# Kernel tuning notes

Measured on AMD Instinct MI355X. Metric: run time of the kernel, lower is better.

Reference implementation:

```python
import jax, jax.numpy as jnp
import numpy as np

B, T, N = 32, 24, 512
DIM_IN, DIM_OUT, HID, EMB = 64, 2, 128, 16
NEG_SLOPE = 0.01  # nn.LeakyReLU default


def leaky_relu(x):
    return jnp.where(x >= 0, x, NEG_SLOPE * x)


def setup_inputs() -> dict:
    key = jax.random.key(0)
    ks = jax.random.split(key, 11)
    return {
        "eb": jax.random.normal(ks[0], (B, T, N, DIM_IN), jnp.float32),
        "time_eb": jax.random.normal(ks[1], (B, T, EMB), jnp.float32),
        "node_eb": jax.random.normal(ks[2], (N, EMB), jnp.float32),
        # ln1: Linear(dim_in, hidden) stored as [dim_in, hidden] (x @ W + b)
        "W1": jax.random.normal(ks[3], (DIM_IN, HID), jnp.float32) / np.sqrt(DIM_IN),
        "b1": jax.random.normal(ks[4], (HID,), jnp.float32) * 0.01,
        # ln3: Linear(hidden, dim_out)
        "W3": jax.random.normal(ks[5], (HID, DIM_OUT), jnp.float32) / np.sqrt(HID),
        "b3": jax.random.normal(ks[6], (DIM_OUT,), jnp.float32) * 0.01,
        "weights_pool_spa": jax.random.normal(ks[7], (EMB, HID, HID), jnp.float32),
        "bias_pool_spa": jax.random.normal(ks[8], (EMB, HID), jnp.float32),
        "weights_pool_tem": jax.random.normal(ks[9], (EMB, HID, HID), jnp.float32),
        "bias_pool_tem": jax.random.normal(ks[10], (EMB, HID), jnp.float32),
    }


def reference(eb, time_eb, node_eb, W1, b1, W3, b3,
              weights_pool_spa, bias_pool_spa,
              weights_pool_tem, bias_pool_tem):
    # eb: [b,t,n,dim_in] -> [b,t,n,hidden]
    eb_out = eb @ W1 + b1
    # spatial hypernetwork: per-node weight [n,hid,hid] and bias [n,hid]
    weights_spa = jnp.einsum('nd,dio->nio', node_eb, weights_pool_spa)
    bias_spa = node_eb @ bias_pool_spa  # [n,hid]
    out_spa = leaky_relu(jnp.einsum('btni,nio->btno', eb_out, weights_spa) + bias_spa)
    # temporal hypernetwork: per-(b,t) weight [b,t,hid,hid] and bias [b,t,1,hid]
    weights_tem = jnp.einsum('btd,dio->btio', time_eb, weights_pool_tem)
    bias_tem = (time_eb @ bias_pool_tem)[:, :, None, :]
    out_tem = leaky_relu(jnp.einsum('btni,btio->btno', out_spa, weights_tem) + bias_tem)
    logits = out_tem @ W3 + b3  # [b,t,n,dim_out]
    return logits
```

## Files before the change

### kernel.cpp

```cpp
#include <hip/hip_runtime.h>
#include <hip/hip_bf16.h>
#include <stdint.h>

#define BT   768
#define NN   512
#define DIN  64
#define HID  128
#define EMB  16
#define SLOPE 0.01f

typedef __attribute__((ext_vector_type(8))) short bf16x8;
typedef __attribute__((ext_vector_type(4))) float f32x4;
typedef __attribute__((ext_vector_type(4))) short short4v;

__device__ __forceinline__ short f2bf(float f) {
    uint32_t u = __float_as_uint(f);
    u += 0x7fff + ((u >> 16) & 1);
    return (short)(u >> 16);
}
__device__ __forceinline__ float bf2f(short s) {
    return __uint_as_float(((uint32_t)(unsigned short)s) << 16);
}

static const size_t OFF_WSPA = 0;
static const size_t OFF_WTEM = 16777216;
static const size_t OFF_BSPA = 41943040;
static const size_t OFF_BTEM = 42205184;
static const size_t OFF_PTS  = 42598400;
static const size_t OFF_PTT  = 43122688;
static const size_t OFF_W1T  = 43646976;
static const size_t OFF_H2   = 43663360;

__global__ __launch_bounds__(256)
void k_prep(const float* __restrict__ pool_spa, const float* __restrict__ pool_tem,
            const float* __restrict__ W1,
            const float* __restrict__ bp_spa, const float* __restrict__ bp_tem,
            const float* __restrict__ node_eb, const float* __restrict__ time_eb,
            short* __restrict__ pts, short* __restrict__ ptt,
            short* __restrict__ w1t, float* __restrict__ bspa,
            float* __restrict__ btem)
{
    const int b = blockIdx.x, t = threadIdx.x;
    if (b >= 129) {
        int q = (b - 129) * 256 + t;
        const float *bp, *emb; float* outp;
        if (q < NN * 32) { bp = bp_spa; emb = node_eb; outp = bspa; }
        else { q -= NN * 32; bp = bp_tem; emb = time_eb; outp = btem; }
        const int n = q >> 5, oq = q & 31;
        float4 a = make_float4(0.f, 0.f, 0.f, 0.f);
        #pragma unroll
        for (int d = 0; d < EMB; ++d) {
            float e = emb[n * EMB + d];
            float4 bv = ((const float4*)bp)[d * 32 + oq];
            a.x += e * bv.x; a.y += e * bv.y; a.z += e * bv.z; a.w += e * bv.w;
        }
        ((float4*)outp)[q] = a;
        return;
    }
    if (b == 128) {
        int o = t >> 1, kh = (t & 1) * 32;
        for (int k = 0; k < 32; ++k)
            w1t[o * 64 + kh + k] = f2bf(W1[(kh + k) * HID + o]);
        return;
    }
    const float* pool = (b < 64) ? pool_spa : pool_tem;
    short* outp = (b < 64) ? pts : ptt;
    const int bb = b & 63;
    const int d = bb >> 2, o0 = (bb & 3) * 32;
    __shared__ short s[32 * 136];
    #pragma unroll
    for (int c = 0; c < 16; ++c) {
        int e = c * 256 + t;
        int i = e >> 5, oo = e & 31;
        s[oo * 136 + i] = f2bf(pool[(d * HID + i) * HID + o0 + oo]);
    }
    __syncthreads();
    #pragma unroll
    for (int c = 0; c < 8; ++c) {
        int e = c * 256 + t;
        int oo = e >> 6, ii = (e & 63) * 2;
        uint32_t lo = (unsigned short)s[oo * 136 + ii];
        uint32_t hi = (unsigned short)s[oo * 136 + ii + 1];
        ((uint32_t*)outp)[((d * HID + o0 + oo) * HID + ii) >> 1] = lo | (hi << 16);
    }
}

__global__ __launch_bounds__(256)
void k_genw(const short* __restrict__ pts, const short* __restrict__ ptt,
            const float* __restrict__ node_eb, const float* __restrict__ time_eb,
            short* __restrict__ wspa, short* __restrict__ wtem)
{
    const int t = threadIdx.x;
    const bool spa = blockIdx.y < 8;
    const int nb = spa ? blockIdx.y : blockIdx.y - 8;
    const short* pool = spa ? pts : ptt;
    const float* emb = spa ? node_eb : time_eb;
    short* outp = spa ? wspa : wtem;
    __shared__ float sEmb[64 * EMB];
    #pragma unroll
    for (int c = 0; c < 4; ++c) {
        int idx = c * 256 + t;
        sEmb[idx] = emb[nb * 64 * EMB + idx];
    }
    __syncthreads();
    const int cq = blockIdx.x * 256 + t;
    float4 p[EMB];
    #pragma unroll
    for (int d = 0; d < EMB; ++d) {
        short4v v = ((const short4v*)pool)[d * 4096 + cq];
        p[d] = make_float4(bf2f(v.x), bf2f(v.y), bf2f(v.z), bf2f(v.w));
    }
    for (int nn = 0; nn < 64; ++nn) {
        float4 a = make_float4(0.f, 0.f, 0.f, 0.f);
        #pragma unroll
        for (int d = 0; d < EMB; ++d) {
            float e = sEmb[nn * EMB + d];
            a.x += e * p[d].x; a.y += e * p[d].y;
            a.z += e * p[d].z; a.w += e * p[d].w;
        }
        short4v o;
        o.x = f2bf(a.x); o.y = f2bf(a.y); o.z = f2bf(a.z); o.w = f2bf(a.w);
        ((short4v*)outp)[(size_t)(nb * 64 + nn) * 4096 + cq] = o;
    }
}

__global__ __launch_bounds__(256)
void k_spatial(const float* __restrict__ eb, const short* __restrict__ w1t,
               const float* __restrict__ b1, const short* __restrict__ wspa,
               const float* __restrict__ bspa, short* __restrict__ h2)
{
    const int n = blockIdx.x, R0 = blockIdx.y * 64;
    const int t = threadIdx.x;
    const int wave = t >> 6, lane = t & 63, quad = lane >> 4, l15 = lane & 15;
    const int m0 = (wave >> 1) * 32, n0 = (wave & 1) * 64;

    __shared__ short sH1[64 * 136];
    __shared__ short sU[128 * 136];
    short* sEb = sU;
    short* sW1 = sU + 64 * 72;
    short* sWs = sU;

    float4 ev[4];
    #pragma unroll
    for (int c = 0; c < 4; ++c) {
        int idx = c * 256 + t;
        int r = idx >> 4, kq = (idx & 15) * 4;
        ev[c] = *(const float4*)(eb + ((size_t)(R0 + r) * NN + n) * DIN + kq);
    }
    bf16x8 w1v[4];
    #pragma unroll
    for (int c = 0; c < 4; ++c) w1v[c] = ((const bf16x8*)w1t)[c * 256 + t];
    float b1r[4], bsr[4];
    #pragma unroll
    for (int tc = 0; tc < 4; ++tc) {
        int col = n0 + tc * 16 + l15;
        b1r[tc] = b1[col];
        bsr[tc] = bspa[n * HID + col];
    }
    bf16x8 wreg[8];
    {
        const bf16x8* src = (const bf16x8*)(wspa + (size_t)n * 16384);
        #pragma unroll
        for (int c = 0; c < 8; ++c) wreg[c] = src[c * 256 + t];
    }
    #pragma unroll
    for (int c = 0; c < 4; ++c) {
        int idx = c * 256 + t;
        int r = idx >> 4, kq = (idx & 15) * 4;
        short4v s;
        s.x = f2bf(ev[c].x); s.y = f2bf(ev[c].y);
        s.z = f2bf(ev[c].z); s.w = f2bf(ev[c].w);
        *(short4v*)(sEb + r * 72 + kq) = s;
    }
    #pragma unroll
    for (int c = 0; c < 4; ++c) {
        int idx = c * 256 + t;
        *(bf16x8*)(sW1 + (idx >> 3) * 72 + (idx & 7) * 8) = w1v[c];
    }
    __syncthreads();

    f32x4 acc1[2][4] = {};
    #pragma unroll
    for (int kc = 0; kc < 2; ++kc) {
        bf16x8 a0 = *(const bf16x8*)(sEb + (m0 + l15) * 72 + kc * 32 + quad * 8);
        bf16x8 a1 = *(const bf16x8*)(sEb + (m0 + 16 + l15) * 72 + kc * 32 + quad * 8);
        #pragma unroll
        for (int tc = 0; tc < 4; ++tc) {
            bf16x8 b = *(const bf16x8*)(sW1 + (n0 + tc * 16 + l15) * 72 + kc * 32 + quad * 8);
            acc1[0][tc] = __builtin_amdgcn_mfma_f32_16x16x32_bf16(a0, b, acc1[0][tc], 0, 0, 0);
            acc1[1][tc] = __builtin_amdgcn_mfma_f32_16x16x32_bf16(a1, b, acc1[1][tc], 0, 0, 0);
        }
    }
    #pragma unroll
    for (int tr = 0; tr < 2; ++tr)
        #pragma unroll
        for (int tc = 0; tc < 4; ++tc) {
            int col = n0 + tc * 16 + l15;
            #pragma unroll
            for (int r = 0; r < 4; ++r)
                sH1[(m0 + tr * 16 + quad * 4 + r) * 136 + col] = f2bf(acc1[tr][tc][r] + b1r[tc]);
        }
    __syncthreads();

    #pragma unroll
    for (int c = 0; c < 8; ++c) {
        int idx = c * 256 + t;
        *(bf16x8*)(sWs + (idx >> 4) * 136 + (idx & 15) * 8) = wreg[c];
    }
    __syncthreads();

    f32x4 acc2[2][4] = {};
    #pragma unroll
    for (int kc = 0; kc < 4; ++kc) {
        bf16x8 a0 = *(const bf16x8*)(sH1 + (m0 + l15) * 136 + kc * 32 + quad * 8);
        bf16x8 a1 = *(const bf16x8*)(sH1 + (m0 + 16 + l15) * 136 + kc * 32 + quad * 8);
        #pragma unroll
        for (int tc = 0; tc < 4; ++tc) {
            bf16x8 b = *(const bf16x8*)(sWs + (n0 + tc * 16 + l15) * 136 + kc * 32 + quad * 8);
            acc2[0][tc] = __builtin_amdgcn_mfma_f32_16x16x32_bf16(a0, b, acc2[0][tc], 0, 0, 0);
            acc2[1][tc] = __builtin_amdgcn_mfma_f32_16x16x32_bf16(a1, b, acc2[1][tc], 0, 0, 0);
        }
    }
    __syncthreads();
    #pragma unroll
    for (int tr = 0; tr < 2; ++tr)
        #pragma unroll
        for (int tc = 0; tc < 4; ++tc) {
            int col = n0 + tc * 16 + l15;
            #pragma unroll
            for (int r = 0; r < 4; ++r) {
                float v = acc2[tr][tc][r] + bsr[tc];
                v = (v >= 0.f) ? v : SLOPE * v;
                sH1[(m0 + tr * 16 + quad * 4 + r) * 136 + col] = f2bf(v);
            }
        }
    __syncthreads();
    #pragma unroll
    for (int c = 0; c < 4; ++c) {
        int idx = c * 256 + t;
        int row = idx >> 4, col = (idx & 15) * 8;
        *(bf16x8*)(h2 + ((size_t)(R0 + row) * NN + n) * HID + col) =
            *(const bf16x8*)(sH1 + row * 136 + col);
    }
}

__global__ __launch_bounds__(256)
void k_temporal(const short* __restrict__ h2, const short* __restrict__ wtem,
                const float* __restrict__ btem, const float* __restrict__ W3,
                const float* __restrict__ b3, float* __restrict__ out)
{
    const int R = blockIdx.x, nbase = blockIdx.y * 256;
    const int t = threadIdx.x;
    const int wave = t >> 6, lane = t & 63, quad = lane >> 4, l15 = lane & 15;
    const int m0 = wave * 16;

    __shared__ short sWt[128 * 136];
    __shared__ short sH2[64 * 136];

    bf16x8 wv[8];
    {
        const bf16x8* src = (const bf16x8*)(wtem + (size_t)R * 16384);
        #pragma unroll
        for (int c = 0; c < 8; ++c) wv[c] = src[c * 256 + t];
    }
    bf16x8 hreg[4];
    {
        const bf16x8* src = (const bf16x8*)(h2 + ((size_t)R * NN + nbase) * HID);
        #pragma unroll
        for (int c = 0; c < 4; ++c) hreg[c] = src[c * 256 + t];
    }
    float btr[8], w3r0[8], w3r1[8];
    #pragma unroll
    for (int tc = 0; tc < 8; ++tc) {
        int o = tc * 16 + l15;
        btr[tc] = btem[R * HID + o];
        w3r0[tc] = W3[2 * o]; w3r1[tc] = W3[2 * o + 1];
    }
    const float b30 = b3[0], b31 = b3[1];

    #pragma unroll
    for (int c = 0; c < 8; ++c) {
        int idx = c * 256 + t;
        *(bf16x8*)(sWt + (idx >> 4) * 136 + (idx & 15) * 8) = wv[c];
    }
    #pragma unroll
    for (int c = 0; c < 4; ++c) {
        int idx = c * 256 + t;
        *(bf16x8*)(sH2 + (idx >> 4) * 136 + (idx & 15) * 8) = hreg[c];
    }
    __syncthreads();

    for (int nt = 0; nt < 4; ++nt) {
        if (nt < 3) {
            const bf16x8* src = (const bf16x8*)(h2 + ((size_t)R * NN + nbase + (nt + 1) * 64) * HID);
            #pragma unroll
            for (int c = 0; c < 4; ++c) hreg[c] = src[c * 256 + t];
        }
        f32x4 acc[8] = {};
        #pragma unroll
        for (int kc = 0; kc < 4; ++kc) {
            bf16x8 a = *(const bf16x8*)(sH2 + (m0 + l15) * 136 + kc * 32 + quad * 8);
            #pragma unroll
            for (int tc = 0; tc < 8; ++tc) {
                bf16x8 b = *(const bf16x8*)(sWt + (tc * 16 + l15) * 136 + kc * 32 + quad * 8);
                acc[tc] = __builtin_amdgcn_mfma_f32_16x16x32_bf16(a, b, acc[tc], 0, 0, 0);
            }
        }
        float pl[4][2] = {};
        #pragma unroll
        for (int tc = 0; tc < 8; ++tc) {
            #pragma unroll
            for (int r = 0; r < 4; ++r) {
                float v = acc[tc][r] + btr[tc];
                v = (v >= 0.f) ? v : SLOPE * v;
                pl[r][0] += v * w3r0[tc];
                pl[r][1] += v * w3r1[tc];
            }
        }
        #pragma unroll
        for (int m = 1; m <= 8; m <<= 1)
            #pragma unroll
            for (int r = 0; r < 4; ++r) {
                pl[r][0] += __shfl_xor(pl[r][0], m);
                pl[r][1] += __shfl_xor(pl[r][1], m);
            }
        if (l15 == 0) {
            #pragma unroll
            for (int r = 0; r < 4; ++r) {
                int nrow = nbase + nt * 64 + m0 + quad * 4 + r;
                *(float2*)(out + ((size_t)R * NN + nrow) * 2) =
                    make_float2(pl[r][0] + b30, pl[r][1] + b31);
            }
        }
        __syncthreads();
        if (nt < 3) {
            #pragma unroll
            for (int c = 0; c < 4; ++c) {
                int idx = c * 256 + t;
                *(bf16x8*)(sH2 + (idx >> 4) * 136 + (idx & 15) * 8) = hreg[c];
            }
            __syncthreads();
        }
    }
}

extern "C" void kernel_launch(void* const* d_in, const int* in_sizes, int n_in,
                              void* d_out, int out_size, void* d_ws, size_t ws_size,
                              hipStream_t stream) {
    const float* eb        = (const float*)d_in[0];
    const float* time_eb   = (const float*)d_in[1];
    const float* node_eb   = (const float*)d_in[2];
    const float* W1        = (const float*)d_in[3];
    const float* b1        = (const float*)d_in[4];
    const float* W3        = (const float*)d_in[5];
    const float* b3        = (const float*)d_in[6];
    const float* pool_spa  = (const float*)d_in[7];
    const float* bpool_spa = (const float*)d_in[8];
    const float* pool_tem  = (const float*)d_in[9];
    const float* bpool_tem = (const float*)d_in[10];
    float* out = (float*)d_out;

    char* ws = (char*)d_ws;
    short* wspa = (short*)(ws + OFF_WSPA);
    short* wtem = (short*)(ws + OFF_WTEM);
    float* bspa = (float*)(ws + OFF_BSPA);
    float* btem = (float*)(ws + OFF_BTEM);
    short* pts  = (short*)(ws + OFF_PTS);
    short* ptt  = (short*)(ws + OFF_PTT);
    short* w1t  = (short*)(ws + OFF_W1T);
    short* h2   = (short*)(ws + OFF_H2);

    k_prep<<<289, 256, 0, stream>>>(pool_spa, pool_tem, W1, bpool_spa, bpool_tem,
                                    node_eb, time_eb, pts, ptt, w1t, bspa, btem);
    k_genw<<<dim3(16, 20), 256, 0, stream>>>(pts, ptt, node_eb, time_eb, wspa, wtem);
    k_spatial<<<dim3(NN, 12), 256, 0, stream>>>(eb, w1t, b1, wspa, bspa, h2);
    k_temporal<<<dim3(BT, 2), 256, 0, stream>>>(h2, wtem, btem, W3, b3, out);
}
```

Before: 241.8 us.

## Fold W1 into spatial hypernetwork pool to remove one GEMM per node

Precomputes W1 multiplied by each spatial pool slice (pool_d^T W1) so the per-node combined weight is a 128x64 matrix, and folds b1 into the spatial bias through a small qtab table. k_spatial then does a single 64-deep MFMA GEMM instead of two chained GEMMs, and the per-node weights it reads are half the size. The cost is an extra prep stage of small GEMMs, plus rounding the product to bf16 before the hypernetwork contraction, which changes numerics slightly.

```diff
diff --git a/kernel.cpp b/kernel.cpp
--- a/kernel.cpp
+++ b/kernel.cpp
@@ -22,27 +22,49 @@
     return __uint_as_float(((uint32_t)(unsigned short)s) << 16);
 }
 
-static const size_t OFF_WSPA = 0;
-static const size_t OFF_WTEM = 16777216;
-static const size_t OFF_BSPA = 41943040;
-static const size_t OFF_BTEM = 42205184;
-static const size_t OFF_PTS  = 42598400;
-static const size_t OFF_PTT  = 43122688;
-static const size_t OFF_W1T  = 43646976;
-static const size_t OFF_H2   = 43663360;
+static const size_t OFF_WCOMB = 0;
+static const size_t OFF_WTEM  = 8388608;
+static const size_t OFF_BSPA  = 33554432;
+static const size_t OFF_BTEM  = 33816576;
+static const size_t OFF_Q     = 34209792;
+static const size_t OFF_PTT   = 34217984;
+static const size_t OFF_PTS2  = 34742272;
+static const size_t OFF_H2    = 35004416;
 
 __global__ __launch_bounds__(256)
 void k_prep(const float* __restrict__ pool_spa, const float* __restrict__ pool_tem,
-            const float* __restrict__ W1,
+            const float* __restrict__ W1, const float* __restrict__ b1,
             const float* __restrict__ bp_spa, const float* __restrict__ bp_tem,
             const float* __restrict__ node_eb, const float* __restrict__ time_eb,
-            short* __restrict__ pts, short* __restrict__ ptt,
-            short* __restrict__ w1t, float* __restrict__ bspa,
+            short* __restrict__ ptt, short* __restrict__ pts2,
+            float* __restrict__ qtab, float* __restrict__ bspa,
             float* __restrict__ btem)
 {
     const int b = blockIdx.x, t = threadIdx.x;
-    if (b >= 129) {
-        int q = (b - 129) * 256 + t;
+    __shared__ short smem[26112];
+
+    if (b < 64) {
+        const int d = b >> 2, o0 = (b & 3) * 32;
+        short* s = smem;
+        #pragma unroll
+        for (int c = 0; c < 16; ++c) {
+            int e = c * 256 + t;
+            int i = e >> 5, oo = e & 31;
+            s[oo * 136 + i] = f2bf(pool_tem[(d * HID + i) * HID + o0 + oo]);
+        }
+        __syncthreads();
+        #pragma unroll
+        for (int c = 0; c < 8; ++c) {
+            int e = c * 256 + t;
+            int oo = e >> 6, ii = (e & 63) * 2;
+            uint32_t lo = (unsigned short)s[oo * 136 + ii];
+            uint32_t hi = (unsigned short)s[oo * 136 + ii + 1];
+            ((uint32_t*)ptt)[((d * HID + o0 + oo) * HID + ii) >> 1] = lo | (hi << 16);
+        }
+        return;
+    }
+    if (b < 224) {
+        int q = (b - 64) * 256 + t;
         const float *bp, *emb; float* outp;
         if (q < NN * 32) { bp = bp_spa; emb = node_eb; outp = bspa; }
         else { q -= NN * 32; bp = bp_tem; emb = time_eb; outp = btem; }
@@ -57,57 +79,98 @@
         ((float4*)outp)[q] = a;
         return;
     }
-    if (b == 128) {
-        int o = t >> 1, kh = (t & 1) * 32;
-        for (int k = 0; k < 32; ++k)
-            w1t[o * 64 + kh + k] = f2bf(W1[(kh + k) * HID + o]);
+    if (b < 226) {
+        const int dbase = (b - 224) * 8;
+        if (t < 128) {
+            float a[8] = {};
+            for (int i = 0; i < HID; ++i) {
+                float bv = b1[i];
+                #pragma unroll
+                for (int dd = 0; dd < 8; ++dd)
+                    a[dd] += bv * pool_spa[((dbase + dd) * HID + i) * HID + t];
+            }
+            #pragma unroll
+            for (int dd = 0; dd < 8; ++dd) qtab[(dbase + dd) * HID + t] = a[dd];
+        }
         return;
     }
-    const float* pool = (b < 64) ? pool_spa : pool_tem;
-    short* outp = (b < 64) ? pts : ptt;
-    const int bb = b & 63;
-    const int d = bb >> 2, o0 = (bb & 3) * 32;
-    __shared__ short s[32 * 136];
-    #pragma unroll
-    for (int c = 0; c < 16; ++c) {
-        int e = c * 256 + t;
-        int i = e >> 5, oo = e & 31;
-        s[oo * 136 + i] = f2bf(pool[(d * HID + i) * HID + o0 + oo]);
+    {
+        const int d = b - 226;
+        const int wave = t >> 6, lane = t & 63, quad = lane >> 4, l15 = lane & 15;
+        const int m0 = wave * 32;
+        short* sPT  = smem;
+        short* sW1b = smem + 128 * 136;
+        #pragma unroll
+        for (int c = 0; c < 64; ++c) {
+            int idx = c * 256 + t;
+            int i = idx >> 7, o = idx & 127;
+            sPT[o * 136 + i] = f2bf(pool_spa[(d * HID + i) * HID + o]);
+        }
+        #pragma unroll
+        for (int c = 0; c < 32; ++c) {
+            int idx = c * 256 + t;
+            sW1b[(idx >> 7) * 136 + (idx & 127)] = f2bf(W1[idx]);
+        }
+        __syncthreads();
+        f32x4 acc[2][4] = {};
+        #pragma unroll
+        for (int kc = 0; kc < 4; ++kc) {
+            bf16x8 a0 = *(const bf16x8*)(sPT + (m0 + l15) * 136 + kc * 32 + quad * 8);
+            bf16x8 a1 = *(const bf16x8*)(sPT + (m0 + 16 + l15) * 136 + kc * 32 + quad * 8);
+            #pragma unroll
+            for (int tc = 0; tc < 4; ++tc) {
+                bf16x8 bb = *(const bf16x8*)(sW1b + (tc * 16 + l15) * 136 + kc * 32 + quad * 8);
+                acc[0][tc] = __builtin_amdgcn_mfma_f32_16x16x32_bf16(a0, bb, acc[0][tc], 0, 0, 0);
+                acc[1][tc] = __builtin_amdgcn_mfma_f32_16x16x32_bf16(a1, bb, acc[1][tc], 0, 0, 0);
+            }
+        }
+        __syncthreads();
+        short* sO = smem;
+        #pragma unroll
+        for (int tr = 0; tr < 2; ++tr)
+            #pragma unroll
+            for (int tc = 0; tc < 4; ++tc)
+                #pragma unroll
+                for (int r = 0; r < 4; ++r)
+                    sO[(m0 + tr * 16 + quad * 4 + r) * 72 + tc * 16 + l15] = f2bf(acc[tr][tc][r]);
+        __syncthreads();
+        #pragma unroll
+        for (int c = 0; c < 4; ++c) {
+            int idx = c * 256 + t;
+            int row = idx >> 3, ko = (idx & 7) * 8;
+            *(bf16x8*)(pts2 + (size_t)d * 8192 + row * 64 + ko) =
+                *(const bf16x8*)(sO + row * 72 + ko);
+        }
+    }
+}
+
+__global__ __launch_bounds__(256)
+void k_genw(const short* __restrict__ pts2, const short* __restrict__ ptt,
+            const float* __restrict__ node_eb, const float* __restrict__ time_eb,
+            short* __restrict__ wcomb, short* __restrict__ wtem)
+{
+    const int t = threadIdx.x, b = blockIdx.x;
+    int nb, cq, stride;
+    const short* pool; const float* emb; short* outp;
+    if (b < 64) {
+        nb = b >> 3; cq = (b & 7) * 256 + t; stride = 2048;
+        pool = pts2; emb = node_eb; outp = wcomb;
+    } else {
+        int bb = b - 64;
+        nb = bb >> 4; cq = (bb & 15) * 256 + t; stride = 4096;
+        pool = ptt; emb = time_eb; outp = wtem;
+    }
+    __shared__ float sEmb[64 * EMB];
+    #pragma unroll
+    for (int c = 0; c < 4; ++c) {
+        int idx = c * 256 + t;
+        sEmb[idx] = emb[nb * 64 * EMB + idx];
     }
     __syncthreads();
-    #pragma unroll
-    for (int c = 0; c < 8; ++c) {
-        int e = c * 256 + t;
-        int oo = e >> 6, ii = (e & 63) * 2;
-        uint32_t lo = (unsigned short)s[oo * 136 + ii];
-        uint32_t hi = (unsigned short)s[oo * 136 + ii + 1];
-        ((uint32_t*)outp)[((d * HID + o0 + oo) * HID + ii) >> 1] = lo | (hi << 16);
-    }
-}
-
-__global__ __launch_bounds__(256)
-void k_genw(const short* __restrict__ pts, const short* __restrict__ ptt,
-            const float* __restrict__ node_eb, const float* __restrict__ time_eb,
-            short* __restrict__ wspa, short* __restrict__ wtem)
-{
-    const int t = threadIdx.x;
-    const bool spa = blockIdx.y < 8;
-    const int nb = spa ? blockIdx.y : blockIdx.y - 8;
-    const short* pool = spa ? pts : ptt;
-    const float* emb = spa ? node_eb : time_eb;
-    short* outp = spa ? wspa : wtem;
-    __shared__ float sEmb[64 * EMB];
-    #pragma unroll
-    for (int c = 0; c < 4; ++c) {
-        int idx = c * 256 + t;
-        sEmb[idx] = emb[nb * 64 * EMB + idx];
-    }
-    __syncthreads();
-    const int cq = blockIdx.x * 256 + t;
     float4 p[EMB];
     #pragma unroll
     for (int d = 0; d < EMB; ++d) {
-        short4v v = ((const short4v*)pool)[d * 4096 + cq];
+        short4v v = ((const short4v*)pool)[d * stride + cq];
         p[d] = make_float4(bf2f(v.x), bf2f(v.y), bf2f(v.z), bf2f(v.w));
     }
     for (int nn = 0; nn < 64; ++nn) {
@@ -120,25 +183,24 @@
         }
         short4v o;
         o.x = f2bf(a.x); o.y = f2bf(a.y); o.z = f2bf(a.z); o.w = f2bf(a.w);
-        ((short4v*)outp)[(size_t)(nb * 64 + nn) * 4096 + cq] = o;
+        ((short4v*)outp)[(size_t)(nb * 64 + nn) * stride + cq] = o;
     }
 }
 
 __global__ __launch_bounds__(256)
-void k_spatial(const float* __restrict__ eb, const short* __restrict__ w1t,
-               const float* __restrict__ b1, const short* __restrict__ wspa,
-               const float* __restrict__ bspa, short* __restrict__ h2)
+void k_spatial(const float* __restrict__ eb, const short* __restrict__ wcomb,
+               const float* __restrict__ bspa, const float* __restrict__ qtab,
+               const float* __restrict__ node_eb, short* __restrict__ h2)
 {
     const int n = blockIdx.x, R0 = blockIdx.y * 64;
     const int t = threadIdx.x;
     const int wave = t >> 6, lane = t & 63, quad = lane >> 4, l15 = lane & 15;
     const int m0 = (wave >> 1) * 32, n0 = (wave & 1) * 64;
 
-    __shared__ short sH1[64 * 136];
-    __shared__ short sU[128 * 136];
-    short* sEb = sU;
-    short* sW1 = sU + 64 * 72;
-    short* sWs = sU;
+    __shared__ short smem[13824];
+    short* sEb  = smem;
+    short* sW   = smem + 64 * 72;
+    short* sOut = smem;
 
     float4 ev[4];
     #pragma unroll
@@ -147,21 +209,21 @@
         int r = idx >> 4, kq = (idx & 15) * 4;
         ev[c] = *(const float4*)(eb + ((size_t)(R0 + r) * NN + n) * DIN + kq);
     }
-    bf16x8 w1v[4];
-    #pragma unroll
-    for (int c = 0; c < 4; ++c) w1v[c] = ((const bf16x8*)w1t)[c * 256 + t];
-    float b1r[4], bsr[4];
+    bf16x8 wreg[4];
+    {
+        const bf16x8* src = (const bf16x8*)(wcomb + (size_t)n * 8192);
+        #pragma unroll
+        for (int c = 0; c < 4; ++c) wreg[c] = src[c * 256 + t];
+    }
+    float bsr[4];
     #pragma unroll
     for (int tc = 0; tc < 4; ++tc) {
         int col = n0 + tc * 16 + l15;
-        b1r[tc] = b1[col];
-        bsr[tc] = bspa[n * HID + col];
-    }
-    bf16x8 wreg[8];
-    {
-        const bf16x8* src = (const bf16x8*)(wspa + (size_t)n * 16384);
-        #pragma unroll
-        for (int c = 0; c < 8; ++c) wreg[c] = src[c * 256 + t];
+        float a = bspa[n * HID + col];
+        #pragma unroll
+        for (int d = 0; d < EMB; ++d)
+            a += node_eb[n * EMB + d] * qtab[d * HID + col];
+        bsr[tc] = a;
     }
     #pragma unroll
     for (int c = 0; c < 4; ++c) {
@@ -175,63 +237,34 @@
     #pragma unroll
     for (int c = 0; c < 4; ++c) {
         int idx = c * 256 + t;
-        *(bf16x8*)(sW1 + (idx >> 3) * 72 + (idx & 7) * 8) = w1v[c];
+        *(bf16x8*)(sW + (idx >> 3) * 72 + (idx & 7) * 8) = wreg[c];
     }
     __syncthreads();
 
-    f32x4 acc1[2][4] = {};
+    f32x4 acc[2][4] = {};
     #pragma unroll
     for (int kc = 0; kc < 2; ++kc) {
         bf16x8 a0 = *(const bf16x8*)(sEb + (m0 + l15) * 72 + kc * 32 + quad * 8);
         bf16x8 a1 = *(const bf16x8*)(sEb + (m0 + 16 + l15) * 72 + kc * 32 + quad * 8);
         #pragma unroll
         for (int tc = 0; tc < 4; ++tc) {
-            bf16x8 b = *(const bf16x8*)(sW1 + (n0 + tc * 16 + l15) * 72 + kc * 32 + quad * 8);
-            acc1[0][tc] = __builtin_amdgcn_mfma_f32_16x16x32_bf16(a0, b, acc1[0][tc], 0, 0, 0);
-            acc1[1][tc] = __builtin_amdgcn_mfma_f32_16x16x32_bf16(a1, b, acc1[1][tc], 0, 0, 0);
-        }
-    }
+            bf16x8 bfr = *(const bf16x8*)(sW + (n0 + tc * 16 + l15) * 72 + kc * 32 + quad * 8);
+            acc[0][tc] = __builtin_amdgcn_mfma_f32_16x16x32_bf16(a0, bfr, acc[0][tc], 0, 0, 0);
+            acc[1][tc] = __builtin_amdgcn_mfma_f32_16x16x32_bf16(a1, bfr, acc[1][tc], 0, 0, 0);
+        }
+    }
+    __syncthreads();
+
     #pragma unroll
     for (int tr = 0; tr < 2; ++tr)
         #pragma unroll
         for (int tc = 0; tc < 4; ++tc) {
             int col = n0 + tc * 16 + l15;
             #pragma unroll
-            for (int r = 0; r < 4; ++r)
-                sH1[(m0 + tr * 16 + quad * 4 + r) * 136 + col] = f2bf(acc1[tr][tc][r] + b1r[tc]);
-        }
-    __syncthreads();
-
-    #pragma unroll
-    for (int c = 0; c < 8; ++c) {
-        int idx = c * 256 + t;
-        *(bf16x8*)(sWs + (idx >> 4) * 136 + (idx & 15) * 8) = wreg[c];
-    }
-    __syncthreads();
-
-    f32x4 acc2[2][4] = {};
-    #pragma unroll
-    for (int kc = 0; kc < 4; ++kc) {
-        bf16x8 a0 = *(const bf16x8*)(sH1 + (m0 + l15) * 136 + kc * 32 + quad * 8);
-        bf16x8 a1 = *(const bf16x8*)(sH1 + (m0 + 16 + l15) * 136 + kc * 32 + quad * 8);
-        #pragma unroll
-        for (int tc = 0; tc < 4; ++tc) {
-            bf16x8 b = *(const bf16x8*)(sWs + (n0 + tc * 16 + l15) * 136 + kc * 32 + quad * 8);
-            acc2[0][tc] = __builtin_amdgcn_mfma_f32_16x16x32_bf16(a0, b, acc2[0][tc], 0, 0, 0);
-            acc2[1][tc] = __builtin_amdgcn_mfma_f32_16x16x32_bf16(a1, b, acc2[1][tc], 0, 0, 0);
-        }
-    }
-    __syncthreads();
-    #pragma unroll
-    for (int tr = 0; tr < 2; ++tr)
-        #pragma unroll
-        for (int tc = 0; tc < 4; ++tc) {
-            int col = n0 + tc * 16 + l15;
-            #pragma unroll
             for (int r = 0; r < 4; ++r) {
-                float v = acc2[tr][tc][r] + bsr[tc];
+                float v = acc[tr][tc][r] + bsr[tc];
                 v = (v >= 0.f) ? v : SLOPE * v;
-                sH1[(m0 + tr * 16 + quad * 4 + r) * 136 + col] = f2bf(v);
+                sOut[(m0 + tr * 16 + quad * 4 + r) * 136 + col] = f2bf(v);
             }
         }
     __syncthreads();
@@ -240,7 +273,7 @@
         int idx = c * 256 + t;
         int row = idx >> 4, col = (idx & 15) * 8;
         *(bf16x8*)(h2 + ((size_t)(R0 + row) * NN + n) * HID + col) =
-            *(const bf16x8*)(sH1 + row * 136 + col);
+            *(const bf16x8*)(sOut + row * 136 + col);
     }
 }
 
@@ -361,18 +394,18 @@
     float* out = (float*)d_out;
 
     char* ws = (char*)d_ws;
-    short* wspa = (short*)(ws + OFF_WSPA);
-    short* wtem = (short*)(ws + OFF_WTEM);
-    float* bspa = (float*)(ws + OFF_BSPA);
-    float* btem = (float*)(ws + OFF_BTEM);
-    short* pts  = (short*)(ws + OFF_PTS);
-    short* ptt  = (short*)(ws + OFF_PTT);
-    short* w1t  = (short*)(ws + OFF_W1T);
-    short* h2   = (short*)(ws + OFF_H2);
-
-    k_prep<<<289, 256, 0, stream>>>(pool_spa, pool_tem, W1, bpool_spa, bpool_tem,
-                                    node_eb, time_eb, pts, ptt, w1t, bspa, btem);
-    k_genw<<<dim3(16, 20), 256, 0, stream>>>(pts, ptt, node_eb, time_eb, wspa, wtem);
-    k_spatial<<<dim3(NN, 12), 256, 0, stream>>>(eb, w1t, b1, wspa, bspa, h2);
+    short* wcomb = (short*)(ws + OFF_WCOMB);
+    short* wtem  = (short*)(ws + OFF_WTEM);
+    float* bspa  = (float*)(ws + OFF_BSPA);
+    float* btem  = (float*)(ws + OFF_BTEM);
+    float* qtab  = (float*)(ws + OFF_Q);
+    short* ptt   = (short*)(ws + OFF_PTT);
+    short* pts2  = (short*)(ws + OFF_PTS2);
+    short* h2    = (short*)(ws + OFF_H2);
+
+    k_prep<<<242, 256, 0, stream>>>(pool_spa, pool_tem, W1, b1, bpool_spa, bpool_tem,
+                                    node_eb, time_eb, ptt, pts2, qtab, bspa, btem);
+    k_genw<<<256, 256, 0, stream>>>(pts2, ptt, node_eb, time_eb, wcomb, wtem);
+    k_spatial<<<dim3(NN, 12), 256, 0, stream>>>(eb, wcomb, bspa, qtab, node_eb, h2);
     k_temporal<<<dim3(BT, 2), 256, 0, stream>>>(h2, wtem, btem, W3, b3, out);
 }
```

After: 257.0 us. +6.3%, slower.
